# Performance work log

Hardware: AMD Instinct MI355X
Metric: run time of the kernel (lower is better)

The kernel has to match this reference:

```python
import jax, jax.numpy as jnp
import numpy as np
import math

B, L, Cs, Cz, Ch, H, Pq, Pv, NB = 1, 768, 384, 128, 16, 12, 4, 8, 30
INF = 100000.0
EPS = 1e-8
HC = H * Ch
CONCAT = H * (Cz + Ch + Pv * 4)


def setup_inputs() -> dict:
    key = jax.random.key(0)
    ks = jax.random.split(key, 24)
    s = jax.random.normal(ks[0], (B, L, Cs), jnp.float32)
    z = jax.random.normal(ks[1], (B, L, NB, Cz), jnp.float32)
    # random orthonormal frames (QR of gaussian) -> valid rigid rotations
    m = jax.random.normal(ks[2], (B, L, 3, 3), jnp.float32)
    rot, _ = jnp.linalg.qr(m)
    trans = jax.random.normal(ks[3], (B, L, 3), jnp.float32) * 10.0
    mask = jnp.ones((B, L), jnp.float32)
    # unique neighbor indices per residue (scatter with duplicate targets is ill-defined)
    E_idx = jnp.argsort(jax.random.uniform(ks[4], (B, L, L)), axis=-1)[..., :NB].astype(jnp.int64)
    sc = 0.02
    W_q = jax.random.normal(ks[5], (Cs, HC), jnp.float32) * sc
    b_q = jnp.zeros((HC,), jnp.float32)
    W_kv = jax.random.normal(ks[6], (Cs, 2 * HC), jnp.float32) * sc
    b_kv = jnp.zeros((2 * HC,), jnp.float32)
    W_qp = jax.random.normal(ks[7], (Cs, H * Pq * 3), jnp.float32) * sc
    b_qp = jnp.zeros((H * Pq * 3,), jnp.float32)
    W_kvp = jax.random.normal(ks[8], (Cs, H * (Pq + Pv) * 3), jnp.float32) * sc
    b_kvp = jnp.zeros((H * (Pq + Pv) * 3,), jnp.float32)
    W_b = jax.random.normal(ks[9], (Cz, H), jnp.float32) * sc
    b_b = jnp.zeros((H,), jnp.float32)
    head_weights = jax.random.normal(ks[10], (H,), jnp.float32) * 0.5 + 0.5
    W_out = jax.random.normal(ks[11], (CONCAT, Cs), jnp.float32) * sc
    b_out = jnp.zeros((Cs,), jnp.float32)
    return dict(s=s, z=z, rot=rot, trans=trans, mask=mask, E_idx=E_idx,
                W_q=W_q, b_q=b_q, W_kv=W_kv, b_kv=b_kv, W_qp=W_qp, b_qp=b_qp,
                W_kvp=W_kvp, b_kvp=b_kvp, W_b=W_b, b_b=b_b,
                head_weights=head_weights, W_out=W_out, b_out=b_out)


def _ipa(s, z, rot, trans, mask, E_idx, W_q, b_q, W_kv, b_kv, W_qp, b_qp,
         W_kvp, b_kvp, W_b, b_b, head_weights, W_out, b_out):
    # scatter neighbor pair features into dense [B, L, L, Cz] (module's z_padding.scatter)
    b_ix = jnp.arange(B)[:, None, None]
    i_ix = jnp.arange(L)[None, :, None]
    z_dense = jnp.zeros((B, L, L, Cz), z.dtype).at[b_ix, i_ix, E_idx].set(z)

    q = (s @ W_q + b_q).reshape(B, L, H, Ch)
    kv = (s @ W_kv + b_kv).reshape(B, L, H, 2 * Ch)
    k, v = kv[..., :Ch], kv[..., Ch:]

    def to_points(flat, P):
        # split into 3 coordinate chunks, stack on last dim -> [B, L, H*P, 3]
        p = jnp.stack(jnp.split(flat, 3, axis=-1), axis=-1)
        # rigid apply: R @ p + t
        p = jnp.einsum('blij,blpj->blpi', rot, p) + trans[:, :, None, :]
        return p.reshape(B, L, H, P, 3)

    q_pts = to_points(s @ W_qp + b_qp, Pq)              # [B,L,H,Pq,3]
    kv_pts = to_points(s @ W_kvp + b_kvp, Pq + Pv)
    k_pts, v_pts = kv_pts[..., :Pq, :], kv_pts[..., Pq:, :]

    bias = z_dense @ W_b + b_b                          # [B,L,L,H]
    a = jnp.einsum('bihc,bjhc->bhij', q, k) * math.sqrt(1.0 / (3 * Ch))
    a = a + math.sqrt(1.0 / 3) * bias.transpose(0, 3, 1, 2)

    # squared point distances [B,L,L,H,Pq]
    diff = q_pts[:, :, None] - k_pts[:, None]           # [B,L,L,H,Pq,3]
    pt_att = jnp.sum(diff * diff, axis=-1)
    hw = jax.nn.softplus(head_weights) * math.sqrt(1.0 / (3 * (Pq * 9.0 / 2)))
    pt_att = jnp.sum(pt_att * hw[None, None, None, :, None], axis=-1) * (-0.5)  # [B,L,L,H]

    sq_mask = INF * (mask[:, :, None] * mask[:, None, :] - 1.0)
    a = a + pt_att.transpose(0, 3, 1, 2) + sq_mask[:, None]
    a = jax.nn.softmax(a, axis=-1)                      # [B,H,L,L]

    o = jnp.einsum('bhij,bjhc->bihc', a, v).reshape(B, L, HC)
    o_pt = jnp.einsum('bhij,bjhpc->bihpc', a, v_pts)    # [B,L,H,Pv,3]
    # rigid invert_apply: R^T (x - t)
    o_pt = jnp.einsum('blji,blhpj->blhpi', rot, o_pt - trans[:, :, None, None, :])
    o_pt_norm = jnp.sqrt(jnp.sum(o_pt ** 2, axis=-1) + EPS).reshape(B, L, H * Pv)
    o_pt = o_pt.reshape(B, L, H * Pv, 3)
    o_pair = jnp.einsum('bhij,bijc->bihc', a, z_dense).reshape(B, L, H * Cz)

    cat = jnp.concatenate(
        [o, o_pt[..., 0], o_pt[..., 1], o_pt[..., 2], o_pt_norm, o_pair], axis=-1)
    return cat @ W_out + b_out


def reference(s, z, rot, trans, mask, E_idx, W_q, b_q, W_kv, b_kv, W_qp, b_qp,
              W_kvp, b_kvp, W_b, b_b, head_weights, W_out, b_out):
    return _ipa(s, z, rot, trans, mask, E_idx, W_q, b_q, W_kv, b_kv, W_qp, b_qp,
                W_kvp, b_kvp, W_b, b_b, head_weights, W_out, b_out)
```

## Files before the change

### kernel.cpp

```cpp
#include <hip/hip_runtime.h>
#include <hip/hip_bf16.h>
#include <math.h>

#define L_    768
#define Cs_   384
#define Cz_   128
#define H_    12
#define NB_   30
#define CONCAT_ 2112
#define PROJN 1152

#define SCALE_QK  0.14433756729740643f
#define SQRT3INV  0.5773502691896258f
#define WC_       0.13608276348795434f
#define INF_      100000.0f

typedef short bf16x8 __attribute__((ext_vector_type(8)));
typedef float f32x4 __attribute__((ext_vector_type(4)));

__device__ __forceinline__ short f2b(float f) {
  __hip_bfloat16 b = __float2bfloat16(f);
  return *reinterpret_cast<short*>(&b);
}
__device__ __forceinline__ float b2f(short s) {
  __hip_bfloat16 b;
  *reinterpret_cast<short*>(&b) = s;
  return __bfloat162float(b);
}

__global__ void pack_kernel(const float* __restrict__ Wq, const float* __restrict__ bq,
                            const float* __restrict__ Wkv, const float* __restrict__ bkv,
                            const float* __restrict__ Wqp, const float* __restrict__ bqp,
                            const float* __restrict__ Wkvp, const float* __restrict__ bkvp,
                            const float* __restrict__ s,
                            short* __restrict__ WallT, float* __restrict__ ball,
                            short* __restrict__ sb) {
  int e = blockIdx.x * 256 + threadIdx.x;
  if (e < Cs_ * PROJN) {
    int col = e / 384, kk = e % 384;
    float v;
    if (col < 192)      v = Wq[kk*192 + col];
    else if (col < 576) v = Wkv[kk*384 + (col-192)];
    else if (col < 720) v = Wqp[kk*144 + (col-576)];
    else                v = Wkvp[kk*432 + (col-720)];
    WallT[e] = f2b(v);
  } else if (e < Cs_ * PROJN + PROJN) {
    int col = e - Cs_ * PROJN;
    float v;
    if (col < 192)      v = bq[col];
    else if (col < 576) v = bkv[col-192];
    else if (col < 720) v = bqp[col-576];
    else                v = bkvp[col-720];
    ball[col] = v;
  } else if (e < Cs_ * PROJN + PROJN + L_ * Cs_) {
    int x = e - (Cs_ * PROJN + PROJN);
    sb[x] = f2b(s[x]);
  }
}

__global__ __launch_bounds__(64) void proj_mfma(const short* __restrict__ A,
                                                const short* __restrict__ Bt,
                                                const float* __restrict__ bias,
                                                float* __restrict__ C) {
  const int l = threadIdx.x, r = l & 15, kg = l >> 4;
  const int m0 = blockIdx.x * 16, n0 = blockIdx.y * 16;
  const short* ap = A  + (size_t)(m0 + r) * 384 + kg * 8;
  const short* bp = Bt + (size_t)(n0 + r) * 384 + kg * 8;
  f32x4 acc = {0.f, 0.f, 0.f, 0.f};
  #pragma unroll
  for (int k = 0; k < 12; ++k) {
    bf16x8 af = *(const bf16x8*)(ap + k * 32);
    bf16x8 bf = *(const bf16x8*)(bp + k * 32);
    acc = __builtin_amdgcn_mfma_f32_16x16x32_bf16(af, bf, acc, 0, 0, 0);
  }
  const float bv = bias[n0 + r];
  #pragma unroll
  for (int j = 0; j < 4; ++j)
    C[(size_t)(m0 + kg * 4 + j) * PROJN + n0 + r] = acc[j] + bv;
}

__global__ __launch_bounds__(256) void prep_kernel(const float* __restrict__ proj,
                                                   const float* __restrict__ rot,
                                                   const float* __restrict__ trans,
                                                   const float* __restrict__ maskp,
                                                   const float* __restrict__ head_w,
                                                   short* __restrict__ Amat,
                                                   short* __restrict__ Bmat,
                                                   short* __restrict__ VmatT,
                                                   float* __restrict__ colbias) {
  const int h = blockIdx.x / 3;
  const int i = (blockIdx.x % 3) * 256 + threadIdx.x;
  const float* p = proj + (size_t)i * PROJN;
  const float* R = rot + i * 9;
  const float* T = trans + i * 3;
  const float c2 = log1pf(expf(head_w[h])) * WC_;
  short* arow = Amat + ((size_t)h * L_ + i) * 64;
  short* brow = Bmat + ((size_t)h * L_ + i) * 64;
  #pragma unroll
  for (int c = 0; c < 16; ++c) {
    arow[c] = f2b(p[h * 16 + c] * SCALE_QK);
    brow[c] = f2b(p[192 + h * 32 + c]);
    VmatT[((size_t)h * 64 + c) * L_ + i] = f2b(p[192 + h * 32 + 16 + c]);
  }
  #pragma unroll
  for (int pt = 0; pt < 4; ++pt) {
    int idx = h * 4 + pt;
    float lx = p[576 + idx], ly = p[576 + 48 + idx], lz = p[576 + 96 + idx];
    float g[3];
    g[0] = R[0]*lx + R[1]*ly + R[2]*lz + T[0];
    g[1] = R[3]*lx + R[4]*ly + R[5]*lz + T[1];
    g[2] = R[6]*lx + R[7]*ly + R[8]*lz + T[2];
    #pragma unroll
    for (int d = 0; d < 3; ++d) {
      float x = c2 * g[d];
      short xh = f2b(x);
      short xl = f2b(x - b2f(xh));
      arow[16 + pt*3 + d] = xh; arow[28 + pt*3 + d] = xh;
      arow[40 + pt*3 + d] = xl; arow[52 + pt*3 + d] = xl;
    }
  }
  float s2 = 0.f;
  #pragma unroll
  for (int pt = 0; pt < 4; ++pt) {
    int idx = h * 12 + pt;
    float lx = p[720 + idx], ly = p[720 + 144 + idx], lz = p[720 + 288 + idx];
    float g[3];
    g[0] = R[0]*lx + R[1]*ly + R[2]*lz + T[0];
    g[1] = R[3]*lx + R[4]*ly + R[5]*lz + T[1];
    g[2] = R[6]*lx + R[7]*ly + R[8]*lz + T[2];
    #pragma unroll
    for (int d = 0; d < 3; ++d) {
      s2 += g[d] * g[d];
      short kh = f2b(g[d]);
      short kl = f2b(g[d] - b2f(kh));
      brow[16 + pt*3 + d] = kh; brow[28 + pt*3 + d] = kl;
      brow[40 + pt*3 + d] = kh; brow[52 + pt*3 + d] = kl;
    }
  }
  colbias[h * L_ + i] = -0.5f * c2 * s2 + INF_ * (maskp[i] - 1.0f);
  #pragma unroll
  for (int pt = 4; pt < 12; ++pt) {
    int idx = h * 12 + pt;
    float lx = p[720 + idx], ly = p[720 + 144 + idx], lz = p[720 + 288 + idx];
    float g[3];
    g[0] = R[0]*lx + R[1]*ly + R[2]*lz + T[0];
    g[1] = R[3]*lx + R[4]*ly + R[5]*lz + T[1];
    g[2] = R[6]*lx + R[7]*ly + R[8]*lz + T[2];
    #pragma unroll
    for (int d = 0; d < 3; ++d) {
      int pc = (pt - 4) * 3 + d;
      short vh = f2b(g[d]);
      short vl = f2b(g[d] - b2f(vh));
      VmatT[((size_t)h * 64 + 16 + pc) * L_ + i] = vh;
      VmatT[((size_t)h * 64 + 40 + pc) * L_ + i] = vl;
    }
  }
}

__global__ __launch_bounds__(64) void bias_mfma(const float* __restrict__ z,
                                                const float* __restrict__ Wb,
                                                float* __restrict__ bias_e) {
  const int l = threadIdx.x, r = l & 15, kg = l >> 4;
  const int m0 = blockIdx.x * 16;
  f32x4 acc = {0.f, 0.f, 0.f, 0.f};
  const float* zr = z + (size_t)(m0 + r) * Cz_ + kg * 8;
  #pragma unroll
  for (int kc = 0; kc < 4; ++kc) {
    float4 a0 = *(const float4*)(zr + kc * 32);
    float4 a1 = *(const float4*)(zr + kc * 32 + 4);
    bf16x8 af, bf;
    af[0]=f2b(a0.x); af[1]=f2b(a0.y); af[2]=f2b(a0.z); af[3]=f2b(a0.w);
    af[4]=f2b(a1.x); af[5]=f2b(a1.y); af[6]=f2b(a1.z); af[7]=f2b(a1.w);
    #pragma unroll
    for (int j = 0; j < 8; ++j) {
      int k = kc * 32 + kg * 8 + j;
      bf[j] = (r < H_) ? f2b(Wb[k * H_ + r]) : (short)0;
    }
    acc = __builtin_amdgcn_mfma_f32_16x16x32_bf16(af, bf, acc, 0, 0, 0);
  }
  if (r < H_) {
    #pragma unroll
    for (int j = 0; j < 4; ++j)
      bias_e[(size_t)(m0 + kg * 4 + j) * H_ + r] = SQRT3INV * acc[j];
  }
}

#define SLS 772
__global__ __launch_bounds__(256) void attn_mfma(
    const short* __restrict__ Amat,
    const short* __restrict__ Bmat,
    const short* __restrict__ VmatT,
    const float* __restrict__ colbias,
    const float* __restrict__ bias_e,
    const int*   __restrict__ E_idx,
    const float* __restrict__ rot,
    const float* __restrict__ trans,
    const float* __restrict__ z,
    short* __restrict__ catb)
{
  const int h = blockIdx.y;
  const int i0 = blockIdx.x * 16;
  const int t = threadIdx.x;
  const int lane = t & 63, wave = t >> 6;
  const int fr = lane & 15, kg = lane >> 4;

  __shared__ __align__(16) float Sl[16][SLS];
  __shared__ float ptb[16][48];
  __shared__ float ews[16][NB_];
  __shared__ int   eidx[16][NB_];
  __shared__ float denom[16];

  const short* Ab = Amat + ((size_t)h * L_ + i0 + fr) * 64 + kg * 8;
  bf16x8 a0 = *(const bf16x8*)(Ab);
  bf16x8 a1 = *(const bf16x8*)(Ab + 32);

  for (int e = t; e < 16 * NB_; e += 256)
    eidx[e / NB_][e % NB_] = E_idx[(i0 + e / NB_) * NB_ + e % NB_];

  #pragma unroll 3
  for (int tt = 0; tt < 12; ++tt) {
    const int j0 = wave * 192 + tt * 16;
    const short* Bb = Bmat + ((size_t)h * L_ + j0 + fr) * 64 + kg * 8;
    f32x4 acc = {0.f, 0.f, 0.f, 0.f};
    acc = __builtin_amdgcn_mfma_f32_16x16x32_bf16(a0, *(const bf16x8*)(Bb), acc, 0, 0, 0);
    acc = __builtin_amdgcn_mfma_f32_16x16x32_bf16(a1, *(const bf16x8*)(Bb + 32), acc, 0, 0, 0);
    const float cb = colbias[h * L_ + j0 + fr];
    #pragma unroll
    for (int j = 0; j < 4; ++j)
      Sl[kg * 4 + j][j0 + fr] = acc[j] + cb;
  }
  __syncthreads();

  for (int e = t; e < 16 * NB_; e += 256) {
    int r = e / NB_, k = e % NB_;
    Sl[r][eidx[r][k]] += bias_e[(size_t)((i0 + r) * NB_ + k) * H_ + h];
  }
  __syncthreads();

  {
    const int r = t >> 4, sub = t & 15;
    float mx = -1e30f;
    #pragma unroll
    for (int n = 0; n < 48; ++n) mx = fmaxf(mx, Sl[r][sub + n * 16]);
    #pragma unroll
    for (int d = 8; d; d >>= 1) mx = fmaxf(mx, __shfl_xor(mx, d, 16));
    float sum = 0.f;
    #pragma unroll
    for (int n = 0; n < 48; ++n) {
      float p = __expf(Sl[r][sub + n * 16] - mx);
      Sl[r][sub + n * 16] = p;
      sum += p;
    }
    #pragma unroll
    for (int d = 8; d; d >>= 1) sum += __shfl_xor(sum, d, 16);
    if (sub == 0) denom[r] = sum;
  }
  __syncthreads();

  for (int e = t; e < 16 * NB_; e += 256) {
    int r = e / NB_, k = e % NB_;
    ews[r][k] = Sl[r][eidx[r][k]];
  }
  {
    const int cr = t & 15;
    const int cc = (t >> 4) * 48;
    float v[48];
    #pragma unroll
    for (int n = 0; n < 12; ++n) {
      float4 u = *(const float4*)&Sl[cr][cc + n * 4];
      v[n*4+0] = u.x; v[n*4+1] = u.y; v[n*4+2] = u.z; v[n*4+3] = u.w;
    }
    __syncthreads();
    unsigned* dst = (unsigned*)&Sl[cr][0];
    #pragma unroll
    for (int n = 0; n < 24; ++n) {
      unsigned lo = (unsigned short)f2b(v[2*n]);
      unsigned hi = (unsigned short)f2b(v[2*n+1]);
      dst[cc/2 + n] = lo | (hi << 16);
    }
  }
  __syncthreads();

  f32x4 oacc = {0.f, 0.f, 0.f, 0.f};
  const short* Vb = VmatT + ((size_t)h * 64 + wave * 16 + fr) * L_ + kg * 8;
  const short* PbRow = (const short*)&Sl[fr][0];
  #pragma unroll 4
  for (int ks = 0; ks < 24; ++ks) {
    bf16x8 pa = *(const bf16x8*)(PbRow + ks * 32 + kg * 8);
    bf16x8 vb = *(const bf16x8*)(Vb + ks * 32);
    oacc = __builtin_amdgcn_mfma_f32_16x16x32_bf16(pa, vb, oacc, 0, 0, 0);
  }
  if (wave == 0) {
    #pragma unroll
    for (int j = 0; j < 4; ++j) {
      int r = kg * 4 + j;
      catb[(size_t)(i0 + r) * CONCAT_ + h * 16 + fr] = f2b(oacc[j] / denom[r]);
    }
  } else {
    int ch = wave * 16 + fr;
    int dest = (ch < 40) ? (ch - 16) : (24 + ch - 40);
    #pragma unroll
    for (int j = 0; j < 4; ++j)
      ptb[kg * 4 + j][dest] = oacc[j];
  }
  __syncthreads();

  if (t < 128) {
    int r = t >> 3, pt = t & 7;
    int ii = i0 + r;
    float di = 1.0f / denom[r];
    const float* T = trans + ii * 3;
    float gx = (ptb[r][pt * 3 + 0] + ptb[r][24 + pt * 3 + 0]) * di - T[0];
    float gy = (ptb[r][pt * 3 + 1] + ptb[r][24 + pt * 3 + 1]) * di - T[1];
    float gz = (ptb[r][pt * 3 + 2] + ptb[r][24 + pt * 3 + 2]) * di - T[2];
    const float* R = rot + ii * 9;
    float lx = R[0] * gx + R[3] * gy + R[6] * gz;
    float ly = R[1] * gx + R[4] * gy + R[7] * gz;
    float lz = R[2] * gx + R[5] * gy + R[8] * gz;
    float nrm = sqrtf(lx * lx + ly * ly + lz * lz + 1e-8f);
    short* crow = catb + (size_t)ii * CONCAT_;
    crow[192 + h * 8 + pt] = f2b(lx);
    crow[288 + h * 8 + pt] = f2b(ly);
    crow[384 + h * 8 + pt] = f2b(lz);
    crow[480 + h * 8 + pt] = f2b(nrm);
  }

  {
    const int r = t >> 4, sub = t & 15;
    const int ii = i0 + r;
    const float di = 1.0f / denom[r];
    float accs[8];
    #pragma unroll
    for (int n = 0; n < 8; ++n) accs[n] = 0.f;
    #pragma unroll 5
    for (int k = 0; k < NB_; ++k) {
      float w = ews[r][k];
      const float* zp = z + ((size_t)ii * NB_ + k) * Cz_ + sub;
      #pragma unroll
      for (int n = 0; n < 8; ++n) accs[n] += w * zp[n * 16];
    }
    short* crow = catb + (size_t)ii * CONCAT_ + 576 + h * Cz_;
    #pragma unroll
    for (int n = 0; n < 8; ++n) crow[sub + n * 16] = f2b(accs[n] * di);
  }
}

__global__ __launch_bounds__(256) void cvt_wout(const float* __restrict__ W, short* __restrict__ Wt) {
  __shared__ float tile[32][33];
  const int k0 = blockIdx.x * 32, n0 = blockIdx.y * 32;
  const int tn = threadIdx.x & 31, tk = threadIdx.x >> 5;
  #pragma unroll
  for (int kk = tk; kk < 32; kk += 8)
    tile[kk][tn] = W[(size_t)(k0 + kk) * Cs_ + n0 + tn];
  __syncthreads();
  #pragma unroll
  for (int rr = tk; rr < 32; rr += 8)
    Wt[(size_t)(n0 + rr) * CONCAT_ + k0 + tn] = f2b(tile[tn][rr]);
}

__global__ __launch_bounds__(256) void gemm_out_mfma(const short* __restrict__ A,
                                                     const short* __restrict__ Bt,
                                                     const float* __restrict__ bias,
                                                     float* __restrict__ C) {
  const int t = threadIdx.x;
  const int w = t >> 6, l = t & 63;
  const int r = l & 15, kg = l >> 4;
  const int m0 = blockIdx.x * 16, n0 = blockIdx.y * 16;
  __shared__ float part[4][16][17];
  const int kcnt = (w < 2) ? 17 : 16;
  const int koff = (w < 2) ? w * 17 : 34 + (w - 2) * 16;
  const short* ap = A  + (size_t)(m0 + r) * CONCAT_ + koff * 32 + kg * 8;
  const short* bp = Bt + (size_t)(n0 + r) * CONCAT_ + koff * 32 + kg * 8;
  f32x4 acc = {0.f, 0.f, 0.f, 0.f};
  #pragma unroll 4
  for (int k = 0; k < kcnt; ++k) {
    bf16x8 af = *(const bf16x8*)(ap + k * 32);
    bf16x8 bf = *(const bf16x8*)(bp + k * 32);
    acc = __builtin_amdgcn_mfma_f32_16x16x32_bf16(af, bf, acc, 0, 0, 0);
  }
  #pragma unroll
  for (int j = 0; j < 4; ++j) part[w][kg * 4 + j][r] = acc[j];
  __syncthreads();
  const int row = t >> 4, col = t & 15;
  float sum = part[0][row][col] + part[1][row][col]
            + part[2][row][col] + part[3][row][col] + bias[n0 + col];
  C[(size_t)(m0 + row) * Cs_ + n0 + col] = sum;
}

extern "C" void kernel_launch(void* const* d_in, const int* in_sizes, int n_in,
                              void* d_out, int out_size, void* d_ws, size_t ws_size,
                              hipStream_t stream) {
  const float* s      = (const float*)d_in[0];
  const float* z      = (const float*)d_in[1];
  const float* rot    = (const float*)d_in[2];
  const float* trans  = (const float*)d_in[3];
  const float* mask   = (const float*)d_in[4];
  const int*   E      = (const int*)  d_in[5];
  const float* W_q    = (const float*)d_in[6];
  const float* b_q    = (const float*)d_in[7];
  const float* W_kv   = (const float*)d_in[8];
  const float* b_kv   = (const float*)d_in[9];
  const float* W_qp   = (const float*)d_in[10];
  const float* b_qp   = (const float*)d_in[11];
  const float* W_kvp  = (const float*)d_in[12];
  const float* b_kvp  = (const float*)d_in[13];
  const float* W_b    = (const float*)d_in[14];
  const float* b_b    = (const float*)d_in[15];  (void)b_b;
  const float* head_w = (const float*)d_in[16];
  const float* W_out  = (const float*)d_in[17];
  const float* b_out  = (const float*)d_in[18];

  float* ws = (float*)d_ws;
  short* WallT   = (short*)(ws + 0);
  float* ball    = ws + 221184;
  short* sb      = (short*)(ws + 222336);
  float* proj    = ws + 369792;
  short* catb    = (short*)(ws + 0);
  short* WoutT   = (short*)(ws + 811008);
  short* Amat    = (short*)(ws + 1254528);
  short* Bmat    = (short*)(ws + 1549440);
  short* VmatT   = (short*)(ws + 1844352);
  float* colbias = ws + 2139264;
  float* bias_e  = ws + 2148480;

  pack_kernel<<<(Cs_ * PROJN + PROJN + L_ * Cs_ + 255) / 256, 256, 0, stream>>>(
      W_q, b_q, W_kv, b_kv, W_qp, b_qp, W_kvp, b_kvp, s, WallT, ball, sb);

  proj_mfma<<<dim3(L_ / 16, PROJN / 16), 64, 0, stream>>>(sb, WallT, ball, proj);

  prep_kernel<<<36, 256, 0, stream>>>(proj, rot, trans, mask, head_w, Amat, Bmat, VmatT, colbias);

  cvt_wout<<<dim3(CONCAT_ / 32, Cs_ / 32), 256, 0, stream>>>(W_out, WoutT);

  bias_mfma<<<(L_ * NB_) / 16, 64, 0, stream>>>(z, W_b, bias_e);

  attn_mfma<<<dim3(L_ / 16, H_), 256, 0, stream>>>(
      Amat, Bmat, VmatT, colbias, bias_e, E, rot, trans, z, catb);

  gemm_out_mfma<<<dim3(L_ / 16, Cs_ / 16), 256, 0, stream>>>(catb, WoutT, b_out, (float*)d_out);
}
```

Measured before the change: 187.2 us.

## Merge preprocessing launches, transpose projection output, and streamline attention softmax

Folds the weight packing, the W_out transpose and the W_b conversion into one preprocess launch, and merges the projection GEMM with the pair-bias GEMM into one launch. This cuts the kernel launch count from seven to five. The projection output is stored transposed so prep_kernel reads coalesced columns, and prep_kernel now uses 128-thread blocks for more parallelism. In attention, softmax packs exponentials directly into bf16 in one pass, gathers neighbour weights from the packed row, reuses the score buffer for point scratch, and sets a waves-per-EU launch bound. The per-neighbour bf16 unpacking adds some ALU work, and the tighter launch bound may force register spills.

```diff
diff --git a/kernel.cpp b/kernel.cpp
--- a/kernel.cpp
+++ b/kernel.cpp
@@ -28,58 +28,115 @@
   return __bfloat162float(b);
 }
 
-__global__ void pack_kernel(const float* __restrict__ Wq, const float* __restrict__ bq,
-                            const float* __restrict__ Wkv, const float* __restrict__ bkv,
-                            const float* __restrict__ Wqp, const float* __restrict__ bqp,
-                            const float* __restrict__ Wkvp, const float* __restrict__ bkvp,
-                            const float* __restrict__ s,
-                            short* __restrict__ WallT, float* __restrict__ ball,
-                            short* __restrict__ sb) {
-  int e = blockIdx.x * 256 + threadIdx.x;
-  if (e < Cs_ * PROJN) {
-    int col = e / 384, kk = e % 384;
-    float v;
-    if (col < 192)      v = Wq[kk*192 + col];
-    else if (col < 576) v = Wkv[kk*384 + (col-192)];
-    else if (col < 720) v = Wqp[kk*144 + (col-576)];
-    else                v = Wkvp[kk*432 + (col-720)];
-    WallT[e] = f2b(v);
-  } else if (e < Cs_ * PROJN + PROJN) {
-    int col = e - Cs_ * PROJN;
-    float v;
-    if (col < 192)      v = bq[col];
-    else if (col < 576) v = bkv[col-192];
-    else if (col < 720) v = bqp[col-576];
-    else                v = bkvp[col-720];
-    ball[col] = v;
-  } else if (e < Cs_ * PROJN + PROJN + L_ * Cs_) {
-    int x = e - (Cs_ * PROJN + PROJN);
-    sb[x] = f2b(s[x]);
-  }
-}
-
-__global__ __launch_bounds__(64) void proj_mfma(const short* __restrict__ A,
-                                                const short* __restrict__ Bt,
-                                                const float* __restrict__ bias,
-                                                float* __restrict__ C) {
+#define PK_E1 (Cs_*PROJN)
+#define PK_E2 (PK_E1 + PROJN)
+#define PK_E3 (PK_E2 + L_*Cs_)
+#define PK_E4 (PK_E3 + H_*Cz_)
+#define PK_BLOCKS ((PK_E4 + 255) / 256)
+__global__ __launch_bounds__(256) void preprocess(
+    const float* __restrict__ Wq, const float* __restrict__ bq,
+    const float* __restrict__ Wkv, const float* __restrict__ bkv,
+    const float* __restrict__ Wqp, const float* __restrict__ bqp,
+    const float* __restrict__ Wkvp, const float* __restrict__ bkvp,
+    const float* __restrict__ s, const float* __restrict__ Wb,
+    const float* __restrict__ Wout,
+    short* __restrict__ WallT, float* __restrict__ ball,
+    short* __restrict__ sb, short* __restrict__ WbT,
+    short* __restrict__ WoutT) {
+  __shared__ float tile[32][33];
+  const int bid = blockIdx.x;
+  if (bid < PK_BLOCKS) {
+    int e = bid * 256 + threadIdx.x;
+    if (e < PK_E1) {
+      int col = e / 384, kk = e % 384;
+      float v;
+      if (col < 192)      v = Wq[kk*192 + col];
+      else if (col < 576) v = Wkv[kk*384 + (col-192)];
+      else if (col < 720) v = Wqp[kk*144 + (col-576)];
+      else                v = Wkvp[kk*432 + (col-720)];
+      WallT[e] = f2b(v);
+    } else if (e < PK_E2) {
+      int col = e - PK_E1;
+      float v;
+      if (col < 192)      v = bq[col];
+      else if (col < 576) v = bkv[col-192];
+      else if (col < 720) v = bqp[col-576];
+      else                v = bkvp[col-720];
+      ball[col] = v;
+    } else if (e < PK_E3) {
+      int x = e - PK_E2;
+      sb[x] = f2b(s[x]);
+    } else if (e < PK_E4) {
+      int x = e - PK_E3;
+      WbT[x] = f2b(Wb[(x & 127) * H_ + (x >> 7)]);
+    }
+  } else {
+    const int b2 = bid - PK_BLOCKS;
+    const int k0 = (b2 % 66) * 32, n0 = (b2 / 66) * 32;
+    const int tn = threadIdx.x & 31, tk = threadIdx.x >> 5;
+    #pragma unroll
+    for (int kk = tk; kk < 32; kk += 8)
+      tile[kk][tn] = Wout[(size_t)(k0 + kk) * Cs_ + n0 + tn];
+    __syncthreads();
+    #pragma unroll
+    for (int rr = tk; rr < 32; rr += 8)
+      WoutT[(size_t)(n0 + rr) * CONCAT_ + k0 + tn] = f2b(tile[tn][rr]);
+  }
+}
+
+__global__ __launch_bounds__(64) void proj_bias_mfma(
+    const short* __restrict__ A,
+    const short* __restrict__ Bt,
+    const float* __restrict__ bias,
+    float* __restrict__ CT,
+    const float* __restrict__ z,
+    const short* __restrict__ WbT,
+    float* __restrict__ bias_e) {
   const int l = threadIdx.x, r = l & 15, kg = l >> 4;
-  const int m0 = blockIdx.x * 16, n0 = blockIdx.y * 16;
-  const short* ap = A  + (size_t)(m0 + r) * 384 + kg * 8;
-  const short* bp = Bt + (size_t)(n0 + r) * 384 + kg * 8;
-  f32x4 acc = {0.f, 0.f, 0.f, 0.f};
-  #pragma unroll
-  for (int k = 0; k < 12; ++k) {
-    bf16x8 af = *(const bf16x8*)(ap + k * 32);
-    bf16x8 bf = *(const bf16x8*)(bp + k * 32);
-    acc = __builtin_amdgcn_mfma_f32_16x16x32_bf16(af, bf, acc, 0, 0, 0);
-  }
-  const float bv = bias[n0 + r];
-  #pragma unroll
-  for (int j = 0; j < 4; ++j)
-    C[(size_t)(m0 + kg * 4 + j) * PROJN + n0 + r] = acc[j] + bv;
-}
-
-__global__ __launch_bounds__(256) void prep_kernel(const float* __restrict__ proj,
+  const int bid = blockIdx.x;
+  if (bid < 3456) {
+    const int m0 = (bid % 48) * 16, n0 = (bid / 48) * 16;
+    const short* ap = A  + (size_t)(m0 + r) * 384 + kg * 8;
+    const short* bp = Bt + (size_t)(n0 + r) * 384 + kg * 8;
+    f32x4 acc = {0.f, 0.f, 0.f, 0.f};
+    #pragma unroll
+    for (int k = 0; k < 12; ++k) {
+      bf16x8 af = *(const bf16x8*)(ap + k * 32);
+      bf16x8 bfv = *(const bf16x8*)(bp + k * 32);
+      acc = __builtin_amdgcn_mfma_f32_16x16x32_bf16(af, bfv, acc, 0, 0, 0);
+    }
+    const float bv = bias[n0 + r];
+    float4 st;
+    st.x = acc[0] + bv; st.y = acc[1] + bv; st.z = acc[2] + bv; st.w = acc[3] + bv;
+    *(float4*)&CT[(size_t)(n0 + r) * L_ + m0 + kg * 4] = st;
+  } else {
+    const int m0 = (bid - 3456) * 16;
+    f32x4 acc = {0.f, 0.f, 0.f, 0.f};
+    const float* zr = z + (size_t)(m0 + r) * Cz_ + kg * 8;
+    #pragma unroll
+    for (int kc = 0; kc < 4; ++kc) {
+      float4 a0 = *(const float4*)(zr + kc * 32);
+      float4 a1 = *(const float4*)(zr + kc * 32 + 4);
+      bf16x8 af, bfv;
+      af[0]=f2b(a0.x); af[1]=f2b(a0.y); af[2]=f2b(a0.z); af[3]=f2b(a0.w);
+      af[4]=f2b(a1.x); af[5]=f2b(a1.y); af[6]=f2b(a1.z); af[7]=f2b(a1.w);
+      if (r < H_) {
+        bfv = *(const bf16x8*)(WbT + r * Cz_ + kc * 32 + kg * 8);
+      } else {
+        #pragma unroll
+        for (int j = 0; j < 8; ++j) bfv[j] = 0;
+      }
+      acc = __builtin_amdgcn_mfma_f32_16x16x32_bf16(af, bfv, acc, 0, 0, 0);
+    }
+    if (r < H_) {
+      #pragma unroll
+      for (int j = 0; j < 4; ++j)
+        bias_e[(size_t)(m0 + kg * 4 + j) * H_ + r] = SQRT3INV * acc[j];
+    }
+  }
+}
+
+__global__ __launch_bounds__(128) void prep_kernel(const float* __restrict__ pT,
                                                    const float* __restrict__ rot,
                                                    const float* __restrict__ trans,
                                                    const float* __restrict__ maskp,
@@ -88,9 +145,9 @@
                                                    short* __restrict__ Bmat,
                                                    short* __restrict__ VmatT,
                                                    float* __restrict__ colbias) {
-  const int h = blockIdx.x / 3;
-  const int i = (blockIdx.x % 3) * 256 + threadIdx.x;
-  const float* p = proj + (size_t)i * PROJN;
+  const int h = blockIdx.x / 6;
+  const int i = (blockIdx.x % 6) * 128 + threadIdx.x;
+  #define PT(c) pT[(size_t)(c) * L_ + i]
   const float* R = rot + i * 9;
   const float* T = trans + i * 3;
   const float c2 = log1pf(expf(head_w[h])) * WC_;
@@ -98,14 +155,14 @@
   short* brow = Bmat + ((size_t)h * L_ + i) * 64;
   #pragma unroll
   for (int c = 0; c < 16; ++c) {
-    arow[c] = f2b(p[h * 16 + c] * SCALE_QK);
-    brow[c] = f2b(p[192 + h * 32 + c]);
-    VmatT[((size_t)h * 64 + c) * L_ + i] = f2b(p[192 + h * 32 + 16 + c]);
+    arow[c] = f2b(PT(h * 16 + c) * SCALE_QK);
+    brow[c] = f2b(PT(192 + h * 32 + c));
+    VmatT[((size_t)h * 64 + c) * L_ + i] = f2b(PT(192 + h * 32 + 16 + c));
   }
   #pragma unroll
   for (int pt = 0; pt < 4; ++pt) {
     int idx = h * 4 + pt;
-    float lx = p[576 + idx], ly = p[576 + 48 + idx], lz = p[576 + 96 + idx];
+    float lx = PT(576 + idx), ly = PT(576 + 48 + idx), lz = PT(576 + 96 + idx);
     float g[3];
     g[0] = R[0]*lx + R[1]*ly + R[2]*lz + T[0];
     g[1] = R[3]*lx + R[4]*ly + R[5]*lz + T[1];
@@ -123,7 +180,7 @@
   #pragma unroll
   for (int pt = 0; pt < 4; ++pt) {
     int idx = h * 12 + pt;
-    float lx = p[720 + idx], ly = p[720 + 144 + idx], lz = p[720 + 288 + idx];
+    float lx = PT(720 + idx), ly = PT(720 + 144 + idx), lz = PT(720 + 288 + idx);
     float g[3];
     g[0] = R[0]*lx + R[1]*ly + R[2]*lz + T[0];
     g[1] = R[3]*lx + R[4]*ly + R[5]*lz + T[1];
@@ -141,7 +198,7 @@
   #pragma unroll
   for (int pt = 4; pt < 12; ++pt) {
     int idx = h * 12 + pt;
-    float lx = p[720 + idx], ly = p[720 + 144 + idx], lz = p[720 + 288 + idx];
+    float lx = PT(720 + idx), ly = PT(720 + 144 + idx), lz = PT(720 + 288 + idx);
     float g[3];
     g[0] = R[0]*lx + R[1]*ly + R[2]*lz + T[0];
     g[1] = R[3]*lx + R[4]*ly + R[5]*lz + T[1];
@@ -155,38 +212,11 @@
       VmatT[((size_t)h * 64 + 40 + pc) * L_ + i] = vl;
     }
   }
-}
-
-__global__ __launch_bounds__(64) void bias_mfma(const float* __restrict__ z,
-                                                const float* __restrict__ Wb,
-                                                float* __restrict__ bias_e) {
-  const int l = threadIdx.x, r = l & 15, kg = l >> 4;
-  const int m0 = blockIdx.x * 16;
-  f32x4 acc = {0.f, 0.f, 0.f, 0.f};
-  const float* zr = z + (size_t)(m0 + r) * Cz_ + kg * 8;
-  #pragma unroll
-  for (int kc = 0; kc < 4; ++kc) {
-    float4 a0 = *(const float4*)(zr + kc * 32);
-    float4 a1 = *(const float4*)(zr + kc * 32 + 4);
-    bf16x8 af, bf;
-    af[0]=f2b(a0.x); af[1]=f2b(a0.y); af[2]=f2b(a0.z); af[3]=f2b(a0.w);
-    af[4]=f2b(a1.x); af[5]=f2b(a1.y); af[6]=f2b(a1.z); af[7]=f2b(a1.w);
-    #pragma unroll
-    for (int j = 0; j < 8; ++j) {
-      int k = kc * 32 + kg * 8 + j;
-      bf[j] = (r < H_) ? f2b(Wb[k * H_ + r]) : (short)0;
-    }
-    acc = __builtin_amdgcn_mfma_f32_16x16x32_bf16(af, bf, acc, 0, 0, 0);
-  }
-  if (r < H_) {
-    #pragma unroll
-    for (int j = 0; j < 4; ++j)
-      bias_e[(size_t)(m0 + kg * 4 + j) * H_ + r] = SQRT3INV * acc[j];
-  }
+  #undef PT
 }
 
 #define SLS 772
-__global__ __launch_bounds__(256) void attn_mfma(
+__global__ __launch_bounds__(256, 3) void attn_mfma(
     const short* __restrict__ Amat,
     const short* __restrict__ Bmat,
     const short* __restrict__ VmatT,
@@ -205,17 +235,16 @@
   const int fr = lane & 15, kg = lane >> 4;
 
   __shared__ __align__(16) float Sl[16][SLS];
-  __shared__ float ptb[16][48];
-  __shared__ float ews[16][NB_];
-  __shared__ int   eidx[16][NB_];
+  __shared__ unsigned short eidx[16][NB_];
   __shared__ float denom[16];
+  #define PTB(r, c) Sl[r][512 + (c)]
 
   const short* Ab = Amat + ((size_t)h * L_ + i0 + fr) * 64 + kg * 8;
   bf16x8 a0 = *(const bf16x8*)(Ab);
   bf16x8 a1 = *(const bf16x8*)(Ab + 32);
 
   for (int e = t; e < 16 * NB_; e += 256)
-    eidx[e / NB_][e % NB_] = E_idx[(i0 + e / NB_) * NB_ + e % NB_];
+    eidx[e / NB_][e % NB_] = (unsigned short)E_idx[(i0 + e / NB_) * NB_ + e % NB_];
 
   #pragma unroll 3
   for (int tt = 0; tt < 12; ++tt) {
@@ -239,45 +268,29 @@
 
   {
     const int r = t >> 4, sub = t & 15;
+    float4 v[12];
+    const float4* src = (const float4*)&Sl[r][sub * 48];
+    #pragma unroll
+    for (int n = 0; n < 12; ++n) v[n] = src[n];
     float mx = -1e30f;
     #pragma unroll
-    for (int n = 0; n < 48; ++n) mx = fmaxf(mx, Sl[r][sub + n * 16]);
+    for (int n = 0; n < 12; ++n)
+      mx = fmaxf(mx, fmaxf(fmaxf(v[n].x, v[n].y), fmaxf(v[n].z, v[n].w)));
     #pragma unroll
     for (int d = 8; d; d >>= 1) mx = fmaxf(mx, __shfl_xor(mx, d, 16));
     float sum = 0.f;
-    #pragma unroll
-    for (int n = 0; n < 48; ++n) {
-      float p = __expf(Sl[r][sub + n * 16] - mx);
-      Sl[r][sub + n * 16] = p;
-      sum += p;
+    unsigned* dst = (unsigned*)&Sl[r][0] + sub * 24;
+    #pragma unroll
+    for (int n = 0; n < 12; ++n) {
+      float e0 = __expf(v[n].x - mx), e1 = __expf(v[n].y - mx);
+      float e2 = __expf(v[n].z - mx), e3 = __expf(v[n].w - mx);
+      sum += (e0 + e1) + (e2 + e3);
+      dst[2*n]   = (unsigned)(unsigned short)f2b(e0) | ((unsigned)(unsigned short)f2b(e1) << 16);
+      dst[2*n+1] = (unsigned)(unsigned short)f2b(e2) | ((unsigned)(unsigned short)f2b(e3) << 16);
     }
     #pragma unroll
     for (int d = 8; d; d >>= 1) sum += __shfl_xor(sum, d, 16);
     if (sub == 0) denom[r] = sum;
-  }
-  __syncthreads();
-
-  for (int e = t; e < 16 * NB_; e += 256) {
-    int r = e / NB_, k = e % NB_;
-    ews[r][k] = Sl[r][eidx[r][k]];
-  }
-  {
-    const int cr = t & 15;
-    const int cc = (t >> 4) * 48;
-    float v[48];
-    #pragma unroll
-    for (int n = 0; n < 12; ++n) {
-      float4 u = *(const float4*)&Sl[cr][cc + n * 4];
-      v[n*4+0] = u.x; v[n*4+1] = u.y; v[n*4+2] = u.z; v[n*4+3] = u.w;
-    }
-    __syncthreads();
-    unsigned* dst = (unsigned*)&Sl[cr][0];
-    #pragma unroll
-    for (int n = 0; n < 24; ++n) {
-      unsigned lo = (unsigned short)f2b(v[2*n]);
-      unsigned hi = (unsigned short)f2b(v[2*n+1]);
-      dst[cc/2 + n] = lo | (hi << 16);
-    }
   }
   __syncthreads();
 
@@ -301,7 +314,7 @@
     int dest = (ch < 40) ? (ch - 16) : (24 + ch - 40);
     #pragma unroll
     for (int j = 0; j < 4; ++j)
-      ptb[kg * 4 + j][dest] = oacc[j];
+      PTB(kg * 4 + j, dest) = oacc[j];
   }
   __syncthreads();
 
@@ -310,9 +323,9 @@
     int ii = i0 + r;
     float di = 1.0f / denom[r];
     const float* T = trans + ii * 3;
-    float gx = (ptb[r][pt * 3 + 0] + ptb[r][24 + pt * 3 + 0]) * di - T[0];
-    float gy = (ptb[r][pt * 3 + 1] + ptb[r][24 + pt * 3 + 1]) * di - T[1];
-    float gz = (ptb[r][pt * 3 + 2] + ptb[r][24 + pt * 3 + 2]) * di - T[2];
+    float gx = (PTB(r, pt * 3 + 0) + PTB(r, 24 + pt * 3 + 0)) * di - T[0];
+    float gy = (PTB(r, pt * 3 + 1) + PTB(r, 24 + pt * 3 + 1)) * di - T[1];
+    float gz = (PTB(r, pt * 3 + 2) + PTB(r, 24 + pt * 3 + 2)) * di - T[2];
     const float* R = rot + ii * 9;
     float lx = R[0] * gx + R[3] * gy + R[6] * gz;
     float ly = R[1] * gx + R[4] * gy + R[7] * gz;
@@ -329,12 +342,15 @@
     const int r = t >> 4, sub = t & 15;
     const int ii = i0 + r;
     const float di = 1.0f / denom[r];
+    const unsigned* Pw = (const unsigned*)&Sl[r][0];
     float accs[8];
     #pragma unroll
     for (int n = 0; n < 8; ++n) accs[n] = 0.f;
     #pragma unroll 5
     for (int k = 0; k < NB_; ++k) {
-      float w = ews[r][k];
+      int j = eidx[r][k];
+      unsigned pw = Pw[j >> 1];
+      float w = b2f((short)((j & 1) ? (pw >> 16) : (pw & 0xffff)));
       const float* zp = z + ((size_t)ii * NB_ + k) * Cz_ + sub;
       #pragma unroll
       for (int n = 0; n < 8; ++n) accs[n] += w * zp[n * 16];
@@ -343,19 +359,7 @@
     #pragma unroll
     for (int n = 0; n < 8; ++n) crow[sub + n * 16] = f2b(accs[n] * di);
   }
-}
-
-__global__ __launch_bounds__(256) void cvt_wout(const float* __restrict__ W, short* __restrict__ Wt) {
-  __shared__ float tile[32][33];
-  const int k0 = blockIdx.x * 32, n0 = blockIdx.y * 32;
-  const int tn = threadIdx.x & 31, tk = threadIdx.x >> 5;
-  #pragma unroll
-  for (int kk = tk; kk < 32; kk += 8)
-    tile[kk][tn] = W[(size_t)(k0 + kk) * Cs_ + n0 + tn];
-  __syncthreads();
-  #pragma unroll
-  for (int rr = tk; rr < 32; rr += 8)
-    Wt[(size_t)(n0 + rr) * CONCAT_ + k0 + tn] = f2b(tile[tn][rr]);
+  #undef PTB
 }
 
 __global__ __launch_bounds__(256) void gemm_out_mfma(const short* __restrict__ A,
@@ -375,8 +379,8 @@
   #pragma unroll 4
   for (int k = 0; k < kcnt; ++k) {
     bf16x8 af = *(const bf16x8*)(ap + k * 32);
-    bf16x8 bf = *(const bf16x8*)(bp + k * 32);
-    acc = __builtin_amdgcn_mfma_f32_16x16x32_bf16(af, bf, acc, 0, 0, 0);
+    bf16x8 bfv = *(const bf16x8*)(bp + k * 32);
+    acc = __builtin_amdgcn_mfma_f32_16x16x32_bf16(af, bfv, acc, 0, 0, 0);
   }
   #pragma unroll
   for (int j = 0; j < 4; ++j) part[w][kg * 4 + j][r] = acc[j];
@@ -414,25 +418,25 @@
   short* WallT   = (short*)(ws + 0);
   float* ball    = ws + 221184;
   short* sb      = (short*)(ws + 222336);
-  float* proj    = ws + 369792;
+  float* projT   = ws + 369792;
   short* catb    = (short*)(ws + 0);
-  short* WoutT   = (short*)(ws + 811008);
   short* Amat    = (short*)(ws + 1254528);
   short* Bmat    = (short*)(ws + 1549440);
   short* VmatT   = (short*)(ws + 1844352);
   float* colbias = ws + 2139264;
   float* bias_e  = ws + 2148480;
-
-  pack_kernel<<<(Cs_ * PROJN + PROJN + L_ * Cs_ + 255) / 256, 256, 0, stream>>>(
-      W_q, b_q, W_kv, b_kv, W_qp, b_qp, W_kvp, b_kvp, s, WallT, ball, sb);
-
-  proj_mfma<<<dim3(L_ / 16, PROJN / 16), 64, 0, stream>>>(sb, WallT, ball, proj);
-
-  prep_kernel<<<36, 256, 0, stream>>>(proj, rot, trans, mask, head_w, Amat, Bmat, VmatT, colbias);
-
-  cvt_wout<<<dim3(CONCAT_ / 32, Cs_ / 32), 256, 0, stream>>>(W_out, WoutT);
-
-  bias_mfma<<<(L_ * NB_) / 16, 64, 0, stream>>>(z, W_b, bias_e);
+  short* WoutT   = (short*)(ws + 2424960);
+  short* WbT     = (short*)(ws + 2830464);
+
+  preprocess<<<PK_BLOCKS + 792, 256, 0, stream>>>(
+      W_q, b_q, W_kv, b_kv, W_qp, b_qp, W_kvp, b_kvp, s, W_b, W_out,
+      WallT, ball, sb, WbT, WoutT);
+
+  proj_bias_mfma<<<3456 + 1440, 64, 0, stream>>>(
+      sb, WallT, ball, projT, z, WbT, bias_e);
+
+  prep_kernel<<<72, 128, 0, stream>>>(projT, rot, trans, mask, head_w,
+                                      Amat, Bmat, VmatT, colbias);
 
   attn_mfma<<<dim3(L_ / 16, H_), 256, 0, stream>>>(
       Amat, Bmat, VmatT, colbias, bias_e, E, rot, trans, z, catb);
```

New measurement: 167.8 us. 10.4% less time.
